# Optimization experiments

Measured on AMD Instinct MI355X. Metric: run time of the kernel, lower is better.

Reference implementation:

```python
import jax, jax.numpy as jnp
import numpy as np

HORIZON = 12
N_LAYERS = 2
HID = 256
DIM = 256
BATCH = 16384


def setup_inputs() -> dict:
    key = jax.random.key(0)
    ks = jax.random.split(key, 8)
    s = 0.05  # keep recurrence well-scaled
    return {
        "y0": jax.random.normal(ks[0], (BATCH, DIM), jnp.float32),
        "h0": jax.random.normal(ks[1], (N_LAYERS, BATCH, HID), jnp.float32),
        "W_ih": jax.random.normal(ks[2], (N_LAYERS, 3 * HID, DIM), jnp.float32) * s,
        "W_hh": jax.random.normal(ks[3], (N_LAYERS, 3 * HID, HID), jnp.float32) * s,
        "b_ih": jax.random.normal(ks[4], (N_LAYERS, 3 * HID), jnp.float32) * s,
        "b_hh": jax.random.normal(ks[5], (N_LAYERS, 3 * HID), jnp.float32) * s,
        "W_lin": jax.random.normal(ks[6], (DIM, HID), jnp.float32) * s,
        "b_lin": jax.random.normal(ks[7], (DIM,), jnp.float32) * s,
    }


def _gru_cell(x, h, Wih, Whh, bih, bhh):
    # torch.nn.GRUCell math
    gi = x @ Wih.T + bih  # [B, 3H]
    gh = h @ Whh.T + bhh  # [B, 3H]
    i_r, i_z, i_n = jnp.split(gi, 3, axis=-1)
    h_r, h_z, h_n = jnp.split(gh, 3, axis=-1)
    r = jax.nn.sigmoid(i_r + h_r)
    z = jax.nn.sigmoid(i_z + h_z)
    n = jnp.tanh(i_n + r * h_n)
    return (1.0 - z) * n + z * h


def reference(y0, h0, W_ih, W_hh, b_ih, b_hh, W_lin, b_lin):
    def step(carry, _):
        ytm1, ht = carry
        x = ytm1
        new_h = []
        for l in range(N_LAYERS):  # small fixed layer count
            hl = _gru_cell(x, ht[l], W_ih[l], W_hh[l], b_ih[l], b_hh[l])
            new_h.append(hl)
            x = hl
        ht = jnp.stack(new_h, axis=0)
        yt = x @ W_lin.T + b_lin  # linear(ht[-1])
        return (yt, ht), yt

    (_, _), yts = jax.lax.scan(step, (y0, h0), None, length=HORIZON)
    # torch.stack(yts, -3) with 2D yt -> [horizon, B, D]
    return yts
```

## Files before the change

kernel.cpp:

```cpp
#include <hip/hip_runtime.h>
#include <hip/hip_bf16.h>
#include <stdint.h>

#define HORIZON 12

typedef __bf16 bf16x8 __attribute__((ext_vector_type(8)));
typedef float  f32x16 __attribute__((ext_vector_type(16)));
typedef float  f32x4v __attribute__((ext_vector_type(4)));

__device__ __forceinline__ unsigned short f2bf(float f) {
  union { float f; uint32_t u; } v; v.f = f;
  return (unsigned short)((v.u + 0x7FFFu + ((v.u >> 16) & 1u)) >> 16);
}
__device__ __forceinline__ float bf2f(unsigned short s) {
  union { uint32_t u; float f; } v; v.u = ((uint32_t)s) << 16;
  return v.f;
}

__device__ __forceinline__ float sigm(float x) { return 1.0f / (1.0f + __expf(-x)); }
__device__ __forceinline__ float tanh_fast(float x) { return 1.0f - 2.0f / (__expf(2.0f * x) + 1.0f); }

#define MFMA(a, b, c) __builtin_amdgcn_mfma_f32_32x32x16_bf16(a, b, c, 0, 0, 0)

__global__ void prep(const float* __restrict__ wih, const float* __restrict__ whh,
                     const float* __restrict__ wlin, const float* __restrict__ bih,
                     const float* __restrict__ bhh, const float* __restrict__ blin,
                     unsigned short* __restrict__ Wb, float* __restrict__ Bc) {
  const int stride = gridDim.x * blockDim.x;
  for (int i = blockIdx.x * blockDim.x + threadIdx.x; i < 215296; i += stride) {
    if (i < 212992) {
      const int e = i << 2;
      const float* src; int m, rel;
      if (e < 196608)      { src = wih + e;             m = 0; rel = e; }
      else if (e < 393216) { src = whh + (e - 196608);  m = 1; rel = e - 196608; }
      else if (e < 589824) { src = wih + (e - 196608);  m = 2; rel = e - 393216; }
      else if (e < 786432) { src = whh + (e - 393216);  m = 3; rel = e - 589824; }
      else                 { src = wlin + (e - 786432); m = 4; rel = e - 786432; }
      const int rows = (m < 4) ? 768 : 256;
      const int r = rel >> 8, c = rel & 255;
      const float4 v = *(const float4*)src;
      unsigned short* dst = Wb + m * 196608 + ((c >> 4) * rows + r) * 16 + (c & 15);
      dst[0] = f2bf(v.x); dst[1] = f2bf(v.y); dst[2] = f2bf(v.z); dst[3] = f2bf(v.w);
    } else {
      const int t = i - 212992;
      float v;
      if (t < 512)       { const int l = t >> 8,        d = t & 255; v = bih[l*768+d]     + bhh[l*768+d]; }
      else if (t < 1024) { const int l = (t-512) >> 8,  d = t & 255; v = bih[l*768+256+d] + bhh[l*768+256+d]; }
      else if (t < 1536) { const int l = (t-1024) >> 8, d = t & 255; v = bih[l*768+512+d]; }
      else if (t < 2048) { const int l = (t-1536) >> 8, d = t & 255; v = bhh[l*768+512+d]; }
      else               { v = blin[t - 2048]; }
      Bc[t] = v;
    }
  }
}

__global__ __launch_bounds__(512) __attribute__((amdgpu_waves_per_eu(2, 2)))
void rnn_persist(
    const float* __restrict__ y0, const float* __restrict__ h0f,
    const unsigned short* __restrict__ Wb, const float* __restrict__ Bc,
    float* __restrict__ out) {
  extern __shared__ char lds[];
  char* XB = lds;
  char* H0 = lds + 32768;
  char* H1 = lds + 65536;

  const int tid = threadIdx.x;
  const int w   = tid >> 6;
  const int l   = tid & 63;
  const int l31 = l & 31;
  const int hi  = l >> 5;
  const int b0  = blockIdx.x * 64;
  const int dw  = w * 32 + l31;
  const int sub2 = (l31 & 7) * 2;
  const int gdw  = w * 4 + (l31 >> 3);

  f32x16 Ar[2], Az[2], Ai[2], Ah[2];

#pragma unroll
  for (int rr = 0; rr < 8; ++rr) {
    const int idx = rr * 2048 + tid * 4;
    const int row = idx >> 8, dd = idx & 255;
    const f32x4v v = __builtin_nontemporal_load(
        (const f32x4v*)(y0 + (size_t)(b0 + row) * 256 + dd));
    ushort4 o; o.x = f2bf(v.x); o.y = f2bf(v.y); o.z = f2bf(v.z); o.w = f2bf(v.w);
    *(ushort4*)(XB + row * 512 + (((dd >> 3) ^ (row & 31)) << 4) + (dd & 7) * 2) = o;
  }

  auto initH = [&](const float* src, char* Hl) {
#pragma unroll
    for (int rr = 0; rr < 8; ++rr) {
      const int idx = rr * 2048 + tid * 4;
      const int row = idx >> 8, dd = idx & 255;
      const f32x4v v = __builtin_nontemporal_load(
          (const f32x4v*)(src + (size_t)(b0 + row) * 256 + dd));
      ushort4 o; o.x = f2bf(v.x); o.y = f2bf(v.y); o.z = f2bf(v.z); o.w = f2bf(v.w);
      *(ushort4*)(Hl + row * 512 + (((dd >> 3) ^ (row & 31)) << 4) + (dd & 7) * 2) = o;
    }
  };
  initH(h0f, H0);
  initH(h0f + (size_t)16384 * 256, H1);
  __syncthreads();

  const char* Wp = (const char*)Wb;

  auto zacc = [&](f32x16 (&A)[2]) {
#pragma unroll
    for (int ct = 0; ct < 2; ++ct)
#pragma unroll
      for (int r = 0; r < 16; ++r) A[ct][r] = 0.0f;
  };

  auto passG3 = [&](const char* As, size_t mBase,
                    f32x16 (&G0)[2], f32x16 (&G1)[2], f32x16 (&G2)[2]) {
    const char* q0 = Wp + mBase + (size_t)(0 * 256 + dw) * 32 + hi * 16;
    const char* q1 = Wp + mBase + (size_t)(1 * 256 + dw) * 32 + hi * 16;
    const char* q2 = Wp + mBase + (size_t)(2 * 256 + dw) * 32 + hi * 16;
    bf16x8 f[3][3];
#define LOADSET3(buf)                                          \
    f[buf][0] = *(const bf16x8*)q0; q0 += 24576;               \
    f[buf][1] = *(const bf16x8*)q1; q1 += 24576;               \
    f[buf][2] = *(const bf16x8*)q2; q2 += 24576;               \
    asm volatile("" : "+v"(q0), "+v"(q1), "+v"(q2));
    LOADSET3(0)
    LOADSET3(1)
#pragma unroll
    for (int k = 0; k < 16; ++k) {
      if (k < 14) { LOADSET3((k + 2) % 3) }
      const int cur = k % 3;
      const int go = ((2 * k + hi) ^ l31) << 4;
      const bf16x8 a0 = *(const bf16x8*)(As + l31 * 512 + go);
      const bf16x8 a1 = *(const bf16x8*)(As + (32 + l31) * 512 + go);
      __builtin_amdgcn_s_setprio(1);
      G0[0] = MFMA(a0, f[cur][0], G0[0]);
      G1[0] = MFMA(a0, f[cur][1], G1[0]);
      G2[0] = MFMA(a0, f[cur][2], G2[0]);
      G0[1] = MFMA(a1, f[cur][0], G0[1]);
      G1[1] = MFMA(a1, f[cur][1], G1[1]);
      G2[1] = MFMA(a1, f[cur][2], G2[1]);
      __builtin_amdgcn_s_setprio(0);
    }
#undef LOADSET3
  };

  auto passLin = [&](const char* Hs, size_t mL) {
    const char* pL = Wp + mL + (size_t)dw * 32 + hi * 16;
    bf16x8 f[3];
    f[0] = *(const bf16x8*)pL; pL += 8192;
    asm volatile("" : "+v"(pL));
    f[1] = *(const bf16x8*)pL; pL += 8192;
    asm volatile("" : "+v"(pL));
#pragma unroll
    for (int k = 0; k < 16; ++k) {
      if (k < 14) {
        f[(k + 2) % 3] = *(const bf16x8*)pL; pL += 8192;
        asm volatile("" : "+v"(pL));
      }
      const int cur = k % 3;
      const int go = ((2 * k + hi) ^ l31) << 4;
      const bf16x8 a0 = *(const bf16x8*)(Hs + l31 * 512 + go);
      const bf16x8 a1 = *(const bf16x8*)(Hs + (32 + l31) * 512 + go);
      __builtin_amdgcn_s_setprio(1);
      Ar[0] = MFMA(a0, f[cur], Ar[0]);
      Ar[1] = MFMA(a1, f[cur], Ar[1]);
      __builtin_amdgcn_s_setprio(0);
    }
  };

  auto epi = [&](int L, char* Hl) {
    const float brz = Bc[L * 256 + dw];
    const float bzz = Bc[512 + L * 256 + dw];
    const float bin = Bc[1024 + L * 256 + dw];
    const float bhn = Bc[1536 + L * 256 + dw];
#pragma unroll
    for (int ct = 0; ct < 2; ++ct) {
#pragma unroll
      for (int reg = 0; reg < 16; ++reg) {
        const int rl = (reg & 3) + 8 * (reg >> 2) + 4 * hi;
        unsigned short* hp =
            (unsigned short*)(Hl + (ct * 32 + rl) * 512 + ((gdw ^ rl) << 4) + sub2);
        const float hold = bf2f(*hp);
        const float rg = sigm(Ar[ct][reg] + brz);
        const float zg = sigm(Az[ct][reg] + bzz);
        const float nn = tanh_fast(Ai[ct][reg] + bin + rg * (Ah[ct][reg] + bhn));
        const float hv = (1.0f - zg) * nn + zg * hold;
        *hp = f2bf(hv);
      }
    }
  };

#pragma unroll 1
  for (int t = 0; t < HORIZON; ++t) {
    {
      const char* wbase = Wp + (size_t)(blockIdx.x >> 3) * 53248;
      uint32_t acc = 0;
#pragma unroll
      for (int j = 0; j < 7; ++j) {
        const int i = j * 512 + tid;
        if (j < 6 || i < 3328) {
          const uint4 wv = *(const uint4*)(wbase + (size_t)i * 16);
          acc ^= wv.x ^ wv.y ^ wv.z ^ wv.w;
        }
      }
      asm volatile("" :: "v"(acc));
    }

    zacc(Ar); zacc(Az); zacc(Ai); zacc(Ah);
    passG3(XB, 0,      Ar, Az, Ai);
    passG3(H0, 393216, Ar, Az, Ah);
    __syncthreads();
    epi(0, H0);
    __syncthreads();
    zacc(Ar); zacc(Az); zacc(Ai); zacc(Ah);
    passG3(H0, 786432,  Ar, Az, Ai);
    passG3(H1, 1179648, Ar, Az, Ah);
    __syncthreads();
    epi(1, H1);
    __syncthreads();
    zacc(Ar);
    passLin(H1, 1572864);
    {
      const float bl = Bc[2048 + dw];
      float* og = out + ((size_t)t * 16384 + b0) * 256;
#pragma unroll
      for (int ct = 0; ct < 2; ++ct) {
#pragma unroll
        for (int reg = 0; reg < 16; ++reg) {
          const int rl = (reg & 3) + 8 * (reg >> 2) + 4 * hi;
          const int row = ct * 32 + rl;
          const float y = Ar[ct][reg] + bl;
          __builtin_nontemporal_store(y, og + (size_t)row * 256 + dw);
          *(unsigned short*)(XB + row * 512 + ((gdw ^ (row & 31)) << 4) + sub2) = f2bf(y);
        }
      }
    }
    __syncthreads();
  }
}

extern "C" void kernel_launch(void* const* d_in, const int* in_sizes, int n_in,
                              void* d_out, int out_size, void* d_ws, size_t ws_size,
                              hipStream_t stream) {
  (void)in_sizes; (void)n_in; (void)out_size; (void)ws_size;
  const float* y0   = (const float*)d_in[0];
  const float* h0   = (const float*)d_in[1];
  const float* wih  = (const float*)d_in[2];
  const float* whh  = (const float*)d_in[3];
  const float* bih  = (const float*)d_in[4];
  const float* bhh  = (const float*)d_in[5];
  const float* wlin = (const float*)d_in[6];
  const float* blin = (const float*)d_in[7];
  float* out = (float*)d_out;

  unsigned short* Wb = (unsigned short*)d_ws;
  float* Bc = (float*)((char*)d_ws + 1703936);

  static bool attr_done = false;
  if (!attr_done) {
    hipFuncSetAttribute((const void*)rnn_persist,
                        hipFuncAttributeMaxDynamicSharedMemorySize, 98304);
    attr_done = true;
  }

  prep<<<512, 256, 0, stream>>>(wih, whh, wlin, bih, bhh, blin, Wb, Bc);
  rnn_persist<<<256, 512, 98304, stream>>>(y0, h0, Wb, Bc, out);
}
```

Measured before the change: 653.7 us.

## Split gate GEMMs into r/z and n passes to cut accumulator registers

Restructures each GRU layer step. The old version ran three-gate passes into four 32-register accumulator sets; the new one runs one pass for the r and z gates (input and hidden contributions summed into two accumulators), turns them into packed bf16 gate values, then runs a second pass for the n gate's input and hidden parts. The aim is to halve accumulator register pressure, and the weight prefetch is deepened from 3 to 4 buffers. It also removes the per-step L2 weight pre-touch loop. In exchange the X/H tiles are read from LDS twice per layer, and r/z are rounded to bf16 before use.

```diff
diff --git a/kernel.cpp b/kernel.cpp
--- a/kernel.cpp
+++ b/kernel.cpp
@@ -74,7 +74,8 @@
   const int sub2 = (l31 & 7) * 2;
   const int gdw  = w * 4 + (l31 >> 3);
 
-  f32x16 Ar[2], Az[2], Ai[2], Ah[2];
+  f32x16 A0[2], A1[2];
+  uint32_t rp[2][8], zp[2][8];
 
 #pragma unroll
   for (int rr = 0; rr < 8; ++rr) {
@@ -103,120 +104,168 @@
 
   const char* Wp = (const char*)Wb;
 
-  auto zacc = [&](f32x16 (&A)[2]) {
+  auto zacc = [&]() {
 #pragma unroll
     for (int ct = 0; ct < 2; ++ct)
 #pragma unroll
-      for (int r = 0; r < 16; ++r) A[ct][r] = 0.0f;
-  };
-
-  auto passG3 = [&](const char* As, size_t mBase,
-                    f32x16 (&G0)[2], f32x16 (&G1)[2], f32x16 (&G2)[2]) {
-    const char* q0 = Wp + mBase + (size_t)(0 * 256 + dw) * 32 + hi * 16;
-    const char* q1 = Wp + mBase + (size_t)(1 * 256 + dw) * 32 + hi * 16;
-    const char* q2 = Wp + mBase + (size_t)(2 * 256 + dw) * 32 + hi * 16;
-    bf16x8 f[3][3];
-#define LOADSET3(buf)                                          \
+      for (int r = 0; r < 16; ++r) { A0[ct][r] = 0.0f; A1[ct][r] = 0.0f; }
+  };
+
+  auto passA = [&](const char* Xs, const char* Hs, size_t mI, size_t mH) {
+    const char* q0 = Wp + mI + (size_t)(0 * 256 + dw) * 32 + hi * 16;
+    const char* q1 = Wp + mI + (size_t)(1 * 256 + dw) * 32 + hi * 16;
+    const char* q2 = Wp + mH + (size_t)(0 * 256 + dw) * 32 + hi * 16;
+    const char* q3 = Wp + mH + (size_t)(1 * 256 + dw) * 32 + hi * 16;
+    bf16x8 f[4][4];
+#define LOADSET4(buf)                                          \
     f[buf][0] = *(const bf16x8*)q0; q0 += 24576;               \
     f[buf][1] = *(const bf16x8*)q1; q1 += 24576;               \
     f[buf][2] = *(const bf16x8*)q2; q2 += 24576;               \
-    asm volatile("" : "+v"(q0), "+v"(q1), "+v"(q2));
-    LOADSET3(0)
-    LOADSET3(1)
+    f[buf][3] = *(const bf16x8*)q3; q3 += 24576;               \
+    asm volatile("" : "+v"(q0), "+v"(q1), "+v"(q2), "+v"(q3));
+    LOADSET4(0)
+    LOADSET4(1)
+    LOADSET4(2)
 #pragma unroll
     for (int k = 0; k < 16; ++k) {
-      if (k < 14) { LOADSET3((k + 2) % 3) }
-      const int cur = k % 3;
+      if (k < 13) { LOADSET4((k + 3) % 4) }
+      const int cur = k % 4;
       const int go = ((2 * k + hi) ^ l31) << 4;
-      const bf16x8 a0 = *(const bf16x8*)(As + l31 * 512 + go);
-      const bf16x8 a1 = *(const bf16x8*)(As + (32 + l31) * 512 + go);
+      const bf16x8 aX0 = *(const bf16x8*)(Xs + l31 * 512 + go);
+      const bf16x8 aH0 = *(const bf16x8*)(Hs + l31 * 512 + go);
+      const bf16x8 aX1 = *(const bf16x8*)(Xs + (32 + l31) * 512 + go);
+      const bf16x8 aH1 = *(const bf16x8*)(Hs + (32 + l31) * 512 + go);
       __builtin_amdgcn_s_setprio(1);
-      G0[0] = MFMA(a0, f[cur][0], G0[0]);
-      G1[0] = MFMA(a0, f[cur][1], G1[0]);
-      G2[0] = MFMA(a0, f[cur][2], G2[0]);
-      G0[1] = MFMA(a1, f[cur][0], G0[1]);
-      G1[1] = MFMA(a1, f[cur][1], G1[1]);
-      G2[1] = MFMA(a1, f[cur][2], G2[1]);
+      A0[0] = MFMA(aX0, f[cur][0], A0[0]);
+      A1[0] = MFMA(aX0, f[cur][1], A1[0]);
+      A0[1] = MFMA(aX1, f[cur][0], A0[1]);
+      A1[1] = MFMA(aX1, f[cur][1], A1[1]);
+      A0[0] = MFMA(aH0, f[cur][2], A0[0]);
+      A1[0] = MFMA(aH0, f[cur][3], A1[0]);
+      A0[1] = MFMA(aH1, f[cur][2], A0[1]);
+      A1[1] = MFMA(aH1, f[cur][3], A1[1]);
       __builtin_amdgcn_s_setprio(0);
     }
-#undef LOADSET3
+#undef LOADSET4
+  };
+
+  auto passB = [&](const char* Xs, const char* Hs, size_t mI, size_t mH) {
+    const char* q0 = Wp + mI + (size_t)(2 * 256 + dw) * 32 + hi * 16;
+    const char* q1 = Wp + mH + (size_t)(2 * 256 + dw) * 32 + hi * 16;
+    bf16x8 f[4][2];
+#define LOADSET2(buf)                                          \
+    f[buf][0] = *(const bf16x8*)q0; q0 += 24576;               \
+    f[buf][1] = *(const bf16x8*)q1; q1 += 24576;               \
+    asm volatile("" : "+v"(q0), "+v"(q1));
+    LOADSET2(0)
+    LOADSET2(1)
+    LOADSET2(2)
+#pragma unroll
+    for (int k = 0; k < 16; ++k) {
+      if (k < 13) { LOADSET2((k + 3) % 4) }
+      const int cur = k % 4;
+      const int go = ((2 * k + hi) ^ l31) << 4;
+      const bf16x8 aX0 = *(const bf16x8*)(Xs + l31 * 512 + go);
+      const bf16x8 aH0 = *(const bf16x8*)(Hs + l31 * 512 + go);
+      const bf16x8 aX1 = *(const bf16x8*)(Xs + (32 + l31) * 512 + go);
+      const bf16x8 aH1 = *(const bf16x8*)(Hs + (32 + l31) * 512 + go);
+      __builtin_amdgcn_s_setprio(1);
+      A0[0] = MFMA(aX0, f[cur][0], A0[0]);
+      A1[0] = MFMA(aH0, f[cur][1], A1[0]);
+      A0[1] = MFMA(aX1, f[cur][0], A0[1]);
+      A1[1] = MFMA(aH1, f[cur][1], A1[1]);
+      __builtin_amdgcn_s_setprio(0);
+    }
+#undef LOADSET2
   };
 
   auto passLin = [&](const char* Hs, size_t mL) {
     const char* pL = Wp + mL + (size_t)dw * 32 + hi * 16;
-    bf16x8 f[3];
-    f[0] = *(const bf16x8*)pL; pL += 8192;
+    bf16x8 f[4];
+#define LOADSET1(buf)                                          \
+    f[buf] = *(const bf16x8*)pL; pL += 8192;                   \
     asm volatile("" : "+v"(pL));
-    f[1] = *(const bf16x8*)pL; pL += 8192;
-    asm volatile("" : "+v"(pL));
+    LOADSET1(0)
+    LOADSET1(1)
+    LOADSET1(2)
 #pragma unroll
     for (int k = 0; k < 16; ++k) {
-      if (k < 14) {
-        f[(k + 2) % 3] = *(const bf16x8*)pL; pL += 8192;
-        asm volatile("" : "+v"(pL));
-      }
-      const int cur = k % 3;
+      if (k < 13) { LOADSET1((k + 3) % 4) }
+      const int cur = k % 4;
       const int go = ((2 * k + hi) ^ l31) << 4;
       const bf16x8 a0 = *(const bf16x8*)(Hs + l31 * 512 + go);
       const bf16x8 a1 = *(const bf16x8*)(Hs + (32 + l31) * 512 + go);
       __builtin_amdgcn_s_setprio(1);
-      Ar[0] = MFMA(a0, f[cur], Ar[0]);
-      Ar[1] = MFMA(a1, f[cur], Ar[1]);
+      A0[0] = MFMA(a0, f[cur], A0[0]);
+      A0[1] = MFMA(a1, f[cur], A0[1]);
       __builtin_amdgcn_s_setprio(0);
     }
-  };
-
-  auto epi = [&](int L, char* Hl) {
+#undef LOADSET1
+  };
+
+  auto epiA = [&](int L) {
     const float brz = Bc[L * 256 + dw];
     const float bzz = Bc[512 + L * 256 + dw];
+#pragma unroll
+    for (int ct = 0; ct < 2; ++ct) {
+#pragma unroll
+      for (int j = 0; j < 8; ++j) {
+        const float r0 = sigm(A0[ct][2 * j]     + brz);
+        const float r1 = sigm(A0[ct][2 * j + 1] + brz);
+        const float z0 = sigm(A1[ct][2 * j]     + bzz);
+        const float z1 = sigm(A1[ct][2 * j + 1] + bzz);
+        rp[ct][j] = (uint32_t)f2bf(r0) | ((uint32_t)f2bf(r1) << 16);
+        zp[ct][j] = (uint32_t)f2bf(z0) | ((uint32_t)f2bf(z1) << 16);
+      }
+    }
+  };
+
+  auto epiB = [&](int L, char* Hl) {
     const float bin = Bc[1024 + L * 256 + dw];
     const float bhn = Bc[1536 + L * 256 + dw];
 #pragma unroll
     for (int ct = 0; ct < 2; ++ct) {
 #pragma unroll
-      for (int reg = 0; reg < 16; ++reg) {
-        const int rl = (reg & 3) + 8 * (reg >> 2) + 4 * hi;
-        unsigned short* hp =
-            (unsigned short*)(Hl + (ct * 32 + rl) * 512 + ((gdw ^ rl) << 4) + sub2);
-        const float hold = bf2f(*hp);
-        const float rg = sigm(Ar[ct][reg] + brz);
-        const float zg = sigm(Az[ct][reg] + bzz);
-        const float nn = tanh_fast(Ai[ct][reg] + bin + rg * (Ah[ct][reg] + bhn));
-        const float hv = (1.0f - zg) * nn + zg * hold;
-        *hp = f2bf(hv);
+      for (int j = 0; j < 8; ++j) {
+#pragma unroll
+        for (int e = 0; e < 2; ++e) {
+          const int reg = 2 * j + e;
+          const float rr = bf2f((unsigned short)(e ? (rp[ct][j] >> 16) : (rp[ct][j] & 0xFFFF)));
+          const float zz = bf2f((unsigned short)(e ? (zp[ct][j] >> 16) : (zp[ct][j] & 0xFFFF)));
+          const int rl = (reg & 3) + 8 * (reg >> 2) + 4 * hi;
+          unsigned short* hp =
+              (unsigned short*)(Hl + (ct * 32 + rl) * 512 + ((gdw ^ rl) << 4) + sub2);
+          const float hold = bf2f(*hp);
+          const float nn = tanh_fast(A0[ct][reg] + bin + rr * (A1[ct][reg] + bhn));
+          const float hv = (1.0f - zz) * nn + zz * hold;
+          *hp = f2bf(hv);
+        }
       }
     }
   };
 
 #pragma unroll 1
   for (int t = 0; t < HORIZON; ++t) {
-    {
-      const char* wbase = Wp + (size_t)(blockIdx.x >> 3) * 53248;
-      uint32_t acc = 0;
-#pragma unroll
-      for (int j = 0; j < 7; ++j) {
-        const int i = j * 512 + tid;
-        if (j < 6 || i < 3328) {
-          const uint4 wv = *(const uint4*)(wbase + (size_t)i * 16);
-          acc ^= wv.x ^ wv.y ^ wv.z ^ wv.w;
-        }
-      }
-      asm volatile("" :: "v"(acc));
-    }
-
-    zacc(Ar); zacc(Az); zacc(Ai); zacc(Ah);
-    passG3(XB, 0,      Ar, Az, Ai);
-    passG3(H0, 393216, Ar, Az, Ah);
-    __syncthreads();
-    epi(0, H0);
-    __syncthreads();
-    zacc(Ar); zacc(Az); zacc(Ai); zacc(Ah);
-    passG3(H0, 786432,  Ar, Az, Ai);
-    passG3(H1, 1179648, Ar, Az, Ah);
-    __syncthreads();
-    epi(1, H1);
-    __syncthreads();
-    zacc(Ar);
+    zacc();
+    passA(XB, H0, 0, 393216);
+    epiA(0);
+    zacc();
+    passB(XB, H0, 0, 393216);
+    __syncthreads();
+    epiB(0, H0);
+    __syncthreads();
+    zacc();
+    passA(H0, H1, 786432, 1179648);
+    epiA(1);
+    zacc();
+    passB(H0, H1, 786432, 1179648);
+    __syncthreads();
+    epiB(1, H1);
+    __syncthreads();
+#pragma unroll
+    for (int ct = 0; ct < 2; ++ct)
+#pragma unroll
+      for (int r = 0; r < 16; ++r) A0[ct][r] = 0.0f;
     passLin(H1, 1572864);
     {
       const float bl = Bc[2048 + dw];
@@ -227,7 +276,7 @@
         for (int reg = 0; reg < 16; ++reg) {
           const int rl = (reg & 3) + 8 * (reg >> 2) + 4 * hi;
           const int row = ct * 32 + rl;
-          const float y = Ar[ct][reg] + bl;
+          const float y = A0[ct][reg] + bl;
           __builtin_nontemporal_store(y, og + (size_t)row * 256 + dw);
           *(unsigned short*)(XB + row * 512 + ((gdw ^ (row & 31)) << 4) + sub2) = f2bf(y);
         }
@@ -256,8 +305,8 @@
 
   static bool attr_done = false;
   if (!attr_done) {
-    hipFuncSetAttribute((const void*)rnn_persist,
-                        hipFuncAttributeMaxDynamicSharedMemorySize, 98304);
+    (void)hipFuncSetAttribute((const void*)rnn_persist,
+                              hipFuncAttributeMaxDynamicSharedMemorySize, 98304);
     attr_done = true;
   }
 
```

Measured after the change: 649.1 us. No clear change (-0.7%).
